# Performance work log

Measured on AMD Instinct MI355X. Metric: run time of the kernel, lower is better.

Reference implementation:

```python
import jax, jax.numpy as jnp
import numpy as np

B, T, J, E, H = 32, 120, 24, 128, 8
d = E // H           # attention_dim = 16
D = J * E            # input_dim = 3072
FF = 256
NEG = -1e9


def _bn(x, g, b):
    # BatchNorm1d over channels-last layout: normalize each of D channels over (batch, time)
    m = x.mean(axis=(0, 1))
    v = x.var(axis=(0, 1))
    return (x - m) * jax.lax.rsqrt(v + 1e-5) * g + b


def setup_inputs() -> dict:
    key = jax.random.key(0)
    ks = jax.random.split(key, 12)
    s = 0.05  # keep activations well-scaled
    return {
        "src_seqs": jax.random.normal(ks[0], (B, T, D), jnp.float32),
        "Wq_t": jax.random.normal(ks[1], (H, J, d, E), jnp.float32) * s,
        "Wk_t": jax.random.normal(ks[2], (H, J, d, E), jnp.float32) * s,
        "Wv_t": jax.random.normal(ks[3], (H, J, d, E), jnp.float32) * s,
        "Wp_t": jax.random.normal(ks[4], (D, D), jnp.float32) * s,
        "bp_t": jnp.zeros((D,), jnp.float32),
        "g_t": jnp.ones((D,), jnp.float32),
        "b_t": jnp.zeros((D,), jnp.float32),
        "Wq_s": jax.random.normal(ks[5], (H, J, d, E), jnp.float32) * s,
        "Wk_s": jax.random.normal(ks[6], (H, d, E), jnp.float32) * s,
        "Wv_s": jax.random.normal(ks[7], (H, d, E), jnp.float32) * s,
        "Wp_s": jax.random.normal(ks[8], (D, D), jnp.float32) * s,
        "bp_s": jnp.zeros((D,), jnp.float32),
        "g_s": jnp.ones((D,), jnp.float32),
        "b_s": jnp.zeros((D,), jnp.float32),
        "W1": jax.random.normal(ks[9], (FF, D), jnp.float32) * s,
        "b1": jnp.zeros((FF,), jnp.float32),
        "W2": jax.random.normal(ks[10], (D, FF), jnp.float32) * s,
        "b2": jnp.zeros((D,), jnp.float32),
        "g_f": jnp.ones((D,), jnp.float32),
        "b_f": jnp.zeros((D,), jnp.float32),
    }


def reference(src_seqs, Wq_t, Wk_t, Wv_t, Wp_t, bp_t, g_t, b_t,
              Wq_s, Wk_s, Wv_s, Wp_s, bp_s, g_s, b_s,
              W1, b1, W2, b2, g_f, b_f):
    Bz, Tz, Dz = src_seqs.shape
    x = src_seqs.reshape(Bz, Tz, J, E)  # per-joint embeddings
    sc = 1.0 / jnp.sqrt(jnp.float32(d))

    # ---- temporal attention (per head h, per joint j; causal over time) ----
    q = jnp.einsum('btje,hjde->bhjtd', x, Wq_t)
    k = jnp.einsum('btje,hjde->bhjtd', x, Wk_t)
    v = jnp.einsum('btje,hjde->bhjtd', x, Wv_t)
    causal = jnp.where(jnp.tril(jnp.ones((Tz, Tz), bool)), 0.0, NEG)
    a = jax.nn.softmax(jnp.einsum('bhjtd,bhjsd->bhjts', q, k) * sc + causal, axis=-1)
    ta = jnp.einsum('bhjts,bhjsd->bhjtd', a, v)
    # concat order: heads outer, joints inner -> (b,t,h,j,d)
    ta = ta.transpose(0, 3, 1, 2, 4).reshape(Bz, Tz, Dz)
    ta = ta @ Wp_t.T + bp_t
    ta = _bn(ta + src_seqs, g_t, b_t)  # dropout=identity (eval)

    # ---- spatial attention (per head h; attends over joints, shared K/V proj) ----
    qs = jnp.einsum('btje,hjde->bhtjd', x, Wq_s)
    ks = jnp.einsum('btje,hde->bhtjd', x, Wk_s)
    vs = jnp.einsum('btje,hde->bhtjd', x, Wv_s)
    asft = jax.nn.softmax(jnp.einsum('bhtjd,bhtkd->bhtjk', qs, ks) * sc, axis=-1)
    sa = jnp.einsum('bhtjk,bhtkd->bhtjd', asft, vs)
    sa = sa.transpose(0, 2, 1, 3, 4).reshape(Bz, Tz, Dz)  # (b,t,h,j,d)
    sa = sa @ Wp_s.T + bp_s
    sa = _bn(sa + src_seqs, g_s, b_s)

    # ---- feed-forward + residual + norm ----
    att = ta + sa
    h1 = jax.nn.relu(att @ W1.T + b1)
    out = _bn((h1 @ W2.T + b2) + att, g_f, b_f)
    return out
```

## Files before the change

kernel.cpp:

```cpp
#include <hip/hip_runtime.h>

typedef unsigned short u16;
typedef __bf16 bf16x8 __attribute__((ext_vector_type(8)));
typedef float f4 __attribute__((ext_vector_type(4)));
typedef float float4v __attribute__((ext_vector_type(4)));
typedef u16 u16x4 __attribute__((ext_vector_type(4)));

#define NX 11796480
#define LDP 136

__device__ __forceinline__ float bf2f(u16 u){ __bf16 h = __builtin_bit_cast(__bf16, u); return (float)h; }
__device__ __forceinline__ u16 f2bf(float f){ __bf16 h = (__bf16)f; return __builtin_bit_cast(u16, h); }

__device__ __forceinline__ void gload_lds16(const u16* g, u16* l){
  __builtin_amdgcn_global_load_lds((const __attribute__((address_space(1))) void*)g,
                                   (__attribute__((address_space(3))) void*)l, 16, 0, 0);
}

__device__ __forceinline__ void cvt4seg(const float* __restrict__ in, u16* __restrict__ out, int i){
  float4v v = *(const float4v*)&in[i*4];
  u16x4 o;
  o[0]=f2bf(v[0]); o[1]=f2bf(v[1]); o[2]=f2bf(v[2]); o[3]=f2bf(v[3]);
  *(u16x4*)&out[i*4] = o;
}

__global__ void k_prep(const float* __restrict__ src, u16* __restrict__ x_bf,
                       const float* __restrict__ wpt, u16* __restrict__ wptb,
                       const float* __restrict__ wps, u16* __restrict__ wpsb,
                       const float* __restrict__ w1,  u16* __restrict__ w1b,
                       const float* __restrict__ w2,  u16* __restrict__ w2b,
                       const float* __restrict__ wqt, const float* __restrict__ wkt,
                       const float* __restrict__ wvt, const float* __restrict__ wqs,
                       const float* __restrict__ wks, const float* __restrict__ wvs,
                       u16* __restrict__ wcat, float* __restrict__ accs){
  int i = blockIdx.x*256 + threadIdx.x;
  if (i < 18432){ accs[i] = 0.f; return; }
  i -= 18432;
  if (i < 2949120){ cvt4seg(src, x_bf, i); return; }
  i -= 2949120;
  if (i < 2359296){ cvt4seg(wpt, wptb, i); return; }
  i -= 2359296;
  if (i < 2359296){ cvt4seg(wps, wpsb, i); return; }
  i -= 2359296;
  if (i < 196608){ cvt4seg(w1, w1b, i); return; }
  i -= 196608;
  if (i < 196608){ cvt4seg(w2, w2b, i); return; }
  i -= 196608;
  int e = i & 127;
  int n = (i >> 7) % 768;
  int j = i / (768*128);
  float v;
  if (n < 512){
    int tn = n >> 7, hh = (n >> 4) & 7, dd = n & 15;
    const float* W = (tn==0)? wqt : (tn==1)? wkt : (tn==2)? wvt : wqs;
    v = W[(((hh*24 + j)*16 + dd) << 7) + e];
  } else {
    int m = n - 512;
    int tn = m >> 7, hh = (m >> 4) & 7, dd = m & 15;
    const float* W = (tn==0)? wks : wvs;
    v = W[((hh*16 + dd) << 7) + e];
  }
  wcat[i] = f2bf(v);
}

__device__ __forceinline__ void gemm_tile(const u16* __restrict__ Ab, int lda,
                                          const u16* __restrict__ Bb, int ldb,
                                          int K, f4 acc[4][4], u16* As, u16* Bs)
{
  const int tid  = threadIdx.x;
  const int lane = tid & 63;
  const int wid  = tid >> 6;
  const int waveM = (wid >> 1) * 64;
  const int waveN = (wid & 1) * 64;
  const int quad = lane >> 4;
  const int r16  = lane & 15;
  const int srow = tid >> 3;
  const int gcol = ((tid & 7) ^ (srow & 7)) * 8;

  #pragma unroll
  for (int mt=0; mt<4; mt++)
    #pragma unroll
    for (int nt=0; nt<4; nt++)
      #pragma unroll
      for (int q=0; q<4; q++) acc[mt][nt][q] = 0.f;

  for (int k0 = 0; k0 < K; k0 += 64){
    __syncthreads();
    #pragma unroll
    for (int i=0; i<4; i++){
      int row = srow + i*32;
      gload_lds16(&Ab[(size_t)row*lda + k0 + gcol], As + wid*512 + i*2048);
      gload_lds16(&Bb[(size_t)row*ldb + k0 + gcol], Bs + wid*512 + i*2048);
    }
    __builtin_amdgcn_s_waitcnt(0);
    __syncthreads();
    #pragma unroll
    for (int kk=0; kk<2; kk++){
      bf16x8 af[4], bfr[4];
      const int soff = ((kk*4 + quad) ^ (r16 & 7)) * 8;
      #pragma unroll
      for (int mt=0; mt<4; mt++)
        af[mt] = *(const bf16x8*)&As[(waveM + mt*16 + r16)*64 + soff];
      #pragma unroll
      for (int nt=0; nt<4; nt++)
        bfr[nt] = *(const bf16x8*)&Bs[(waveN + nt*16 + r16)*64 + soff];
      #pragma unroll
      for (int mt=0; mt<4; mt++)
        #pragma unroll
        for (int nt=0; nt<4; nt++)
          acc[mt][nt] = __builtin_amdgcn_mfma_f32_16x16x32_bf16(af[mt], bfr[nt], acc[mt][nt], 0, 0, 0);
    }
  }
  __syncthreads();
}

__global__ __launch_bounds__(256)
void gemm_qkv(const u16* __restrict__ x, const u16* __restrict__ wcat,
              u16* __restrict__ qt, u16* __restrict__ kt, u16* __restrict__ vt,
              u16* __restrict__ qs, u16* __restrict__ ks, u16* __restrict__ vs)
{
  __shared__ __align__(16) u16 As[128*128];
  __shared__ __align__(16) u16 Bs[128*128];
  int m0 = blockIdx.x*128, j = blockIdx.y;
  const u16* Ab = x + (size_t)m0*3072 + j*128;
  const u16* Bbase = wcat + (size_t)j*98304;
  int tid = threadIdx.x, lane = tid & 63, wid = tid >> 6;
  int quad = lane >> 4, r16 = lane & 15;
  int srow16 = tid >> 4;
  int cslot  = tid & 15;
  int gcol   = (cslot ^ srow16) * 8;

  #pragma unroll
  for (int it=0; it<8; it++){
    int row = srow16 + it*16;
    gload_lds16(&Ab[(size_t)row*3072 + gcol], As + tid*8 + it*2048);
  }

  int waveM = (wid>>1)*64, waveN = (wid&1)*64;

  for (int nc=0; nc<6; nc++){
    const u16* Bb = Bbase + (size_t)(nc*128)*128;
    #pragma unroll
    for (int it=0; it<8; it++){
      int row = srow16 + it*16;
      gload_lds16(&Bb[(size_t)row*128 + gcol], Bs + tid*8 + it*2048);
    }
    __builtin_amdgcn_s_waitcnt(0);
    __syncthreads();

    f4 acc[4][4];
    #pragma unroll
    for (int mt=0; mt<4; mt++)
      #pragma unroll
      for (int nt=0; nt<4; nt++)
        #pragma unroll
        for (int q=0; q<4; q++) acc[mt][nt][q] = 0.f;

    #pragma unroll
    for (int kk=0; kk<4; kk++){
      bf16x8 af[4], bfr[4];
      const int soff = ((kk*4 + quad) ^ r16) * 8;
      #pragma unroll
      for (int mt=0; mt<4; mt++)
        af[mt] = *(const bf16x8*)&As[(waveM + mt*16 + r16)*128 + soff];
      #pragma unroll
      for (int nt=0; nt<4; nt++)
        bfr[nt] = *(const bf16x8*)&Bs[(waveN + nt*16 + r16)*128 + soff];
      #pragma unroll
      for (int mt=0; mt<4; mt++)
        #pragma unroll
        for (int nt=0; nt<4; nt++)
          acc[mt][nt] = __builtin_amdgcn_mfma_f32_16x16x32_bf16(af[mt], bfr[nt], acc[mt][nt], 0, 0, 0);
    }

    #pragma unroll
    for (int mt=0; mt<4; mt++){
      #pragma unroll
      for (int reg=0; reg<4; reg++){
        int row = m0 + waveM + mt*16 + quad*4 + reg;
        int b = row / 120, t = row % 120;
        #pragma unroll
        for (int nt=0; nt<4; nt++){
          int n = nc*128 + waveN + nt*16 + r16;
          u16 uv = f2bf(acc[mt][nt][reg]);
          if (n < 384){
            int tn = n >> 7, hh = (n >> 4) & 7, dd = n & 15;
            u16* base = (tn==0)? qt : (tn==1)? kt : vt;
            base[((((size_t)(b*8+hh)*24 + j)*120 + t) << 4) + dd] = uv;
          } else {
            int m2 = n - 384;
            int tn = m2 >> 7, hh = (m2 >> 4) & 7, dd = m2 & 15;
            u16* base = (tn==0)? qs : (tn==1)? ks : vs;
            base[((((size_t)row*8 + hh)*24 + j) << 4) + dd] = uv;
          }
        }
      }
    }
    __syncthreads();
  }
}


__device__ __forceinline__ void stageA384(const u16* __restrict__ g, int kcol,
                                          u16* __restrict__ slotA, int lane, int wid){
  #pragma unroll
  for (int i=0;i<2;i++){
    int row = wid*32 + i*16 + (lane>>2);
    int sw  = (((lane & 3) ^ ((lane>>3) & 3)) << 3);
    gload_lds16(&g[(size_t)row*3072 + kcol + sw], slotA + (wid*2+i)*512);
  }
}
__device__ __forceinline__ void stageB384(const u16* __restrict__ g, int kcol,
                                          u16* __restrict__ slotB, int lane, int wid){
  #pragma unroll
  for (int i=0;i<3;i++){
    int row = wid*48 + i*16 + (lane>>2);
    int sw  = (((lane & 3) ^ ((lane>>3) & 3)) << 3);
    gload_lds16(&g[(size_t)row*3072 + kcol + sw], slotB + (wid*3+i)*512);
  }
}

__global__ __launch_bounds__(512, 2)
void gemm_proj384(const u16* __restrict__ A0, const u16* __restrict__ B0, const float* __restrict__ b0,
                  const u16* __restrict__ A1, const u16* __restrict__ B1, const float* __restrict__ b1v,
                  const u16* __restrict__ resb, u16* __restrict__ O0, u16* __restrict__ O1,
                  float* __restrict__ st0, float* __restrict__ st1)
{
  __shared__ __align__(16) u16 smem[61440];
  const int tid = threadIdx.x, lane = tid & 63, wid = tid >> 6;
  const int quad = lane >> 4, r16 = lane & 15;
  const int wm = wid >> 2, wn = wid & 3;

  int lin = blockIdx.x + 15*blockIdx.y + 120*blockIdx.z;
  int nidx = (lin & 7)*30 + (lin >> 3);
  int zz = nidx / 120; int rem = nidx - zz*120;
  int by = rem / 15, bx = rem - by*15;

  const int m0 = bx*256, n0 = by*384;
  const u16* Ag = (zz ? A1 : A0) + (size_t)m0*3072;
  const u16* Bg = (zz ? B1 : B0) + (size_t)n0*3072;
  const float* bias = zz ? b1v : b0;
  u16* out = zz ? O1 : O0;
  float* stp = zz ? st1 : st0;

  const int soff = ((quad ^ ((r16>>1)&3)) << 3);
  const int arow = wm*128 + r16;
  const int brow = wn*96 + r16;

  f4 acc[8][6];
  #pragma unroll
  for (int i=0;i<8;i++)
    #pragma unroll
    for (int n=0;n<6;n++)
      #pragma unroll
      for (int q=0;q<4;q++) acc[i][n][q] = 0.f;

  u16* Sa = smem;
  u16* Sb = smem + 20480;
  u16* Sc = smem + 40960;

  stageA384(Ag, 0,  Sa,        lane, wid);
  stageB384(Bg, 0,  Sa + 8192, lane, wid);
  stageA384(Ag, 32, Sb,        lane, wid);
  stageB384(Bg, 32, Sb + 8192, lane, wid);
  asm volatile("s_waitcnt vmcnt(5)" ::: "memory");
  __builtin_amdgcn_s_barrier();

  const int NT = 96;
  bf16x8 af[4], bf[6];

  for (int t=0; t<NT; ++t){
    const int kc2 = ((t+2 < NT) ? (t+2) : 0) * 32;

    #pragma unroll
    for (int i=0;i<4;i++) af[i] = *(const bf16x8*)&Sa[(arow + i*16)*32 + soff];
    #pragma unroll
    for (int n=0;n<6;n++) bf[n] = *(const bf16x8*)&Sa[8192 + (brow + n*16)*32 + soff];
    stageA384(Ag, kc2, Sc, lane, wid);
    __builtin_amdgcn_s_setprio(1);
    #pragma unroll
    for (int i=0;i<4;i++)
      #pragma unroll
      for (int n=0;n<6;n++)
        acc[i][n] = __builtin_amdgcn_mfma_f32_16x16x32_bf16(af[i], bf[n], acc[i][n], 0,0,0);
    __builtin_amdgcn_s_setprio(0);

    #pragma unroll
    for (int i=0;i<4;i++) af[i] = *(const bf16x8*)&Sa[(arow + 64 + i*16)*32 + soff];
    stageB384(Bg, kc2, Sc + 8192, lane, wid);
    __builtin_amdgcn_s_setprio(1);
    #pragma unroll
    for (int i=0;i<4;i++)
      #pragma unroll
      for (int n=0;n<6;n++)
        acc[4+i][n] = __builtin_amdgcn_mfma_f32_16x16x32_bf16(af[i], bf[n], acc[4+i][n], 0,0,0);
    __builtin_amdgcn_s_setprio(0);

    asm volatile("s_waitcnt vmcnt(5)" ::: "memory");
    __builtin_amdgcn_s_barrier();
    u16* tp = Sa; Sa = Sb; Sb = Sc; Sc = tp;
  }
  asm volatile("s_waitcnt vmcnt(0)" ::: "memory");

  float bv[6];
  #pragma unroll
  for (int n=0;n<6;n++) bv[n] = bias[n0 + wn*96 + n*16 + r16];
  float s[6] = {0,0,0,0,0,0}, s2[6] = {0,0,0,0,0,0};
  #pragma unroll
  for (int mf=0; mf<8; mf++){
    #pragma unroll
    for (int reg=0; reg<4; reg++){
      int grow = m0 + wm*128 + mf*16 + quad*4 + reg;
      #pragma unroll
      for (int n=0;n<6;n++){
        int gcol = n0 + wn*96 + n*16 + r16;
        size_t idx = (size_t)grow*3072 + gcol;
        float v = acc[mf][n][reg] + bv[n] + bf2f(resb[idx]);
        out[idx] = f2bf(v);
        s[n] += v; s2[n] += v*v;
      }
    }
  }
  #pragma unroll
  for (int n=0;n<6;n++){
    float a = s[n], b = s2[n];
    a += __shfl_xor(a, 16); a += __shfl_xor(a, 32);
    b += __shfl_xor(b, 16); b += __shfl_xor(b, 32);
    if (quad == 0){
      int col = n0 + wn*96 + n*16 + r16;
      atomicAdd(&stp[col], a);
      atomicAdd(&stp[3072 + col], b);
    }
  }
}

__global__ __launch_bounds__(256)
void gemm_ff2(const u16* __restrict__ A, const u16* __restrict__ B, const float* __restrict__ bias,
              const u16* __restrict__ resb, u16* __restrict__ out, float* __restrict__ stp)
{
  __shared__ __align__(16) u16 As[128*64];
  __shared__ __align__(16) u16 Bs[128*64];
  int m0 = blockIdx.x*128, n0 = blockIdx.y*128;
  f4 acc[4][4];
  gemm_tile(A + (size_t)m0*256, 256, B + (size_t)n0*256, 256, 256, acc, As, Bs);
  int lane = threadIdx.x & 63, wid = threadIdx.x >> 6;
  int waveM = (wid>>1)*64, waveN = (wid&1)*64;
  int quad = lane>>4, r16 = lane&15;
  float s[4] = {0,0,0,0}, s2[4] = {0,0,0,0};
  #pragma unroll
  for (int mt=0; mt<4; mt++){
    #pragma unroll
    for (int reg=0; reg<4; reg++){
      int grow = m0 + waveM + mt*16 + quad*4 + reg;
      #pragma unroll
      for (int nt=0; nt<4; nt++){
        int gcol = n0 + waveN + nt*16 + r16;
        size_t idx = (size_t)grow*3072 + gcol;
        float v = acc[mt][nt][reg] + bias[gcol] + bf2f(resb[idx]);
        out[idx] = f2bf(v);
        s[nt] += v; s2[nt] += v*v;
      }
    }
  }
  #pragma unroll
  for (int nt=0; nt<4; nt++){
    float a = s[nt], b = s2[nt];
    a += __shfl_xor(a, 16); a += __shfl_xor(a, 32);
    b += __shfl_xor(b, 16); b += __shfl_xor(b, 32);
    if (quad == 0){
      int col = n0 + waveN + nt*16 + r16;
      atomicAdd(&stp[col], a);
      atomicAdd(&stp[3072 + col], b);
    }
  }
}

__global__ __launch_bounds__(256)
void gemm_relu(const u16* __restrict__ A, const u16* __restrict__ B, int K, int N,
               const float* __restrict__ bias, u16* __restrict__ out)
{
  __shared__ __align__(16) u16 As[128*64];
  __shared__ __align__(16) u16 Bs[128*64];
  int m0 = blockIdx.x*128, n0 = blockIdx.y*128;
  f4 acc[4][4];
  gemm_tile(A + (size_t)m0*K, K, B + (size_t)n0*K, K, K, acc, As, Bs);
  int lane = threadIdx.x & 63, wid = threadIdx.x >> 6;
  int waveM = (wid>>1)*64, waveN = (wid&1)*64;
  int quad = lane>>4, r16 = lane&15;
  #pragma unroll
  for (int mt=0; mt<4; mt++){
    #pragma unroll
    for (int reg=0; reg<4; reg++){
      int grow = m0 + waveM + mt*16 + quad*4 + reg;
      #pragma unroll
      for (int nt=0; nt<4; nt++){
        int gcol = n0 + waveN + nt*16 + r16;
        float v = acc[mt][nt][reg] + bias[gcol];
        out[(size_t)grow*N + gcol] = f2bf(v > 0.f ? v : 0.f);
      }
    }
  }
}

__global__ __launch_bounds__(256)
void attn_both(const u16* __restrict__ qt, const u16* __restrict__ kt,
               const u16* __restrict__ vt, u16* __restrict__ ta,
               const u16* __restrict__ qsp, const u16* __restrict__ ksp,
               const u16* __restrict__ vsp, u16* __restrict__ sa)
{
  __shared__ __align__(16) char smem[39168];
  int tid = threadIdx.x, lane = tid & 63, wid = tid >> 6;
  int quad = lane >> 4, r16 = lane & 15;

  if (blockIdx.x < 6144){
    u16* P  = (u16*)smem;
    u16* Vt = (u16*)(smem + 34816);
    int blk = blockIdx.x;
    int b = blk / 192;
    int rem = blk % 192;
    int h = rem / 24, j = rem % 24;
    const u16* qb = qt + (size_t)blk*1920;
    const u16* kb = kt + (size_t)blk*1920;
    const u16* vb = vt + (size_t)blk*1920;

    for (int e = tid; e < 1920; e += 256){
      int s = e >> 4, dd = e & 15;
      Vt[dd*LDP + s] = vb[e];
    }
    if (tid < 128){ int dd = tid >> 3, s = 120 + (tid & 7); Vt[dd*LDP + s] = 0; }
    __syncthreads();

    bf16x8 zv;
    #pragma unroll
    for (int i=0;i<8;i++) zv[i] = (__bf16)0.f;

    const int m0 = wid * 32;
    bf16x8 qf[2];
    #pragma unroll
    for (int mt=0; mt<2; mt++){
      int row = m0 + mt*16 + r16; if (row > 119) row = 119;
      qf[mt] = (quad < 2) ? *(const bf16x8*)&qb[row*16 + (quad&1)*8] : zv;
    }

    f4 S[2][8];
    #pragma unroll
    for (int nt=0; nt<8; nt++){
      int col = nt*16 + r16; int colc = col > 119 ? 119 : col;
      bf16x8 kf = (quad < 2) ? *(const bf16x8*)&kb[colc*16 + (quad&1)*8] : zv;
      #pragma unroll
      for (int mt=0; mt<2; mt++){
        f4 zz = {0.f, 0.f, 0.f, 0.f};
        S[mt][nt] = __builtin_amdgcn_mfma_f32_16x16x32_bf16(qf[mt], kf, zz, 0, 0, 0);
      }
    }

    #pragma unroll
    for (int mt=0; mt<2; mt++)
      #pragma unroll
      for (int nt=0; nt<8; nt++)
        #pragma unroll
        for (int reg=0; reg<4; reg++){
          int c = nt*16 + r16;
          int r = m0 + mt*16 + quad*4 + reg;
          float v = S[mt][nt][reg] * 0.25f;
          S[mt][nt][reg] = (c > r || c >= 120) ? -1e30f : v;
        }

    float Zr[2][4];
    #pragma unroll
    for (int mt=0; mt<2; mt++)
      #pragma unroll
      for (int reg=0; reg<4; reg++){
        float m = -1e30f;
        #pragma unroll
        for (int nt=0; nt<8; nt++) m = fmaxf(m, S[mt][nt][reg]);
        #pragma unroll
        for (int off=1; off<16; off<<=1) m = fmaxf(m, __shfl_xor(m, off, 16));
        float z = 0.f;
        #pragma unroll
        for (int nt=0; nt<8; nt++){
          float e = __expf(S[mt][nt][reg] - m);
          S[mt][nt][reg] = e;
          z += e;
        }
        #pragma unroll
        for (int off=1; off<16; off<<=1) z += __shfl_xor(z, off, 16);
        Zr[mt][reg] = z;
      }

    #pragma unroll
    for (int mt=0; mt<2; mt++)
      #pragma unroll
      for (int nt=0; nt<8; nt++)
        #pragma unroll
        for (int reg=0; reg<4; reg++)
          P[(m0 + mt*16 + quad*4 + reg)*LDP + nt*16 + r16] = f2bf(S[mt][nt][reg]);
    __syncthreads();

    f4 O[2];
    #pragma unroll
    for (int mt=0; mt<2; mt++){ O[mt][0]=0.f; O[mt][1]=0.f; O[mt][2]=0.f; O[mt][3]=0.f; }
    #pragma unroll
    for (int kt8=0; kt8<4; kt8++){
      bf16x8 vf = *(const bf16x8*)&Vt[r16*LDP + kt8*32 + quad*8];
      #pragma unroll
      for (int mt=0; mt<2; mt++){
        bf16x8 pf = *(const bf16x8*)&P[(m0 + mt*16 + r16)*LDP + kt8*32 + quad*8];
        O[mt] = __builtin_amdgcn_mfma_f32_16x16x32_bf16(pf, vf, O[mt], 0, 0, 0);
      }
    }

    #pragma unroll
    for (int mt=0; mt<2; mt++)
      #pragma unroll
      for (int reg=0; reg<4; reg++){
        int r = m0 + mt*16 + quad*4 + reg;
        if (r < 120){
          size_t idx = (size_t)(b*120 + r)*3072 + h*384 + j*16 + r16;
          ta[idx] = f2bf(O[mt][reg] / Zr[mt][reg]);
        }
      }
  } else {
    float* Ks = (float*)smem;
    float* Vs = (float*)(smem + 12288);
    int bt = blockIdx.x - 6144;
    size_t base = (size_t)bt * 3072;
    for (int c = tid; c < 384; c += 256){
      bf16x8 kv = *(const bf16x8*)&ksp[base + c*8];
      bf16x8 vv = *(const bf16x8*)&vsp[base + c*8];
      #pragma unroll
      for (int i=0;i<8;i++){ Ks[c*8+i] = (float)kv[i]; Vs[c*8+i] = (float)vv[i]; }
    }
    __syncthreads();
    if (tid < 192){
      int h = tid / 24, j = tid % 24;
      float q[16];
      #pragma unroll
      for (int d2=0; d2<16; d2++) q[d2] = bf2f(qsp[base + h*384 + j*16 + d2]);
      float sc[24], mx = -1e30f;
      #pragma unroll
      for (int kk=0; kk<24; kk++){
        float dot = 0.f;
        #pragma unroll
        for (int d2=0; d2<16; d2++) dot += q[d2]*Ks[h*384 + kk*16 + d2];
        sc[kk] = dot * 0.25f;
        mx = fmaxf(mx, sc[kk]);
      }
      float Z = 0.f, acc[16];
      #pragma unroll
      for (int d2=0; d2<16; d2++) acc[d2] = 0.f;
      #pragma unroll
      for (int kk=0; kk<24; kk++){
        float w = __expf(sc[kk] - mx);
        Z += w;
        #pragma unroll
        for (int d2=0; d2<16; d2++) acc[d2] += w*Vs[h*384 + kk*16 + d2];
      }
      float inv = 1.f / Z;
      #pragma unroll
      for (int d2=0; d2<16; d2++) sa[base + h*384 + j*16 + d2] = f2bf(acc[d2]*inv);
    }
  }
}

__global__ void bn_coef2(const float* __restrict__ accT, const float* __restrict__ gT,
                         const float* __restrict__ bT, float* __restrict__ cT,
                         const float* __restrict__ accS, const float* __restrict__ gS,
                         const float* __restrict__ bS, float* __restrict__ cS){
  int isS = blockIdx.x >= 12;
  const float* acc = isS ? accS : accT;
  const float* g   = isS ? gS : gT;
  const float* b   = isS ? bS : bT;
  float* coef      = isS ? cS : cT;
  int c = (blockIdx.x % 12)*256 + threadIdx.x;
  float mean = acc[c] * (1.f/3840.f);
  float var  = acc[3072+c] * (1.f/3840.f) - mean*mean;
  float sc = g[c] * rsqrtf(var + 1e-5f);
  coef[c] = sc;
  coef[3072+c] = b[c] - mean*sc;
}

__global__ void bn_coef(const float* __restrict__ acc, const float* __restrict__ g,
                        const float* __restrict__ b, float* __restrict__ coef){
  int c = blockIdx.x*256 + threadIdx.x;
  float mean = acc[c] * (1.f/3840.f);
  float var  = acc[3072+c] * (1.f/3840.f) - mean*mean;
  float sc = g[c] * rsqrtf(var + 1e-5f);
  coef[c] = sc;
  coef[3072+c] = b[c] - mean*sc;
}

__global__ void bn_apply2(const u16* __restrict__ Ytb, const u16* __restrict__ Ysb,
                          const float* __restrict__ ct, const float* __restrict__ cs,
                          u16* __restrict__ attB){
  int i = blockIdx.x*256 + threadIdx.x;
  int c = (i*4) % 3072;
  u16x4 yt = *(const u16x4*)&Ytb[i*4];
  u16x4 ys = *(const u16x4*)&Ysb[i*4];
  u16x4 o;
  #pragma unroll
  for (int k=0;k<4;k++){
    float a = bf2f(yt[k])*ct[c+k] + ct[3072+c+k] + bf2f(ys[k])*cs[c+k] + cs[3072+c+k];
    o[k] = f2bf(a);
  }
  *(u16x4*)&attB[i*4] = o;
}

__global__ void bn_out(const u16* __restrict__ Yfb, const float* __restrict__ cf,
                       float* __restrict__ out){
  int i = blockIdx.x*256 + threadIdx.x;
  int c = (i*4) % 3072;
  u16x4 yf = *(const u16x4*)&Yfb[i*4];
  float4v o;
  #pragma unroll
  for (int k=0;k<4;k++) o[k] = bf2f(yf[k])*cf[c+k] + cf[3072+c+k];
  *(float4v*)&out[i*4] = o;
}

extern "C" void kernel_launch(void* const* d_in, const int* in_sizes, int n_in,
                              void* d_out, int out_size, void* d_ws, size_t ws_size,
                              hipStream_t stream)
{
  const float* src  = (const float*)d_in[0];
  const float* Wq_t = (const float*)d_in[1];
  const float* Wk_t = (const float*)d_in[2];
  const float* Wv_t = (const float*)d_in[3];
  const float* Wp_t = (const float*)d_in[4];
  const float* bp_t = (const float*)d_in[5];
  const float* g_t  = (const float*)d_in[6];
  const float* b_t  = (const float*)d_in[7];
  const float* Wq_s = (const float*)d_in[8];
  const float* Wk_s = (const float*)d_in[9];
  const float* Wv_s = (const float*)d_in[10];
  const float* Wp_s = (const float*)d_in[11];
  const float* bp_s = (const float*)d_in[12];
  const float* g_s  = (const float*)d_in[13];
  const float* b_s  = (const float*)d_in[14];
  const float* W1   = (const float*)d_in[15];
  const float* b1   = (const float*)d_in[16];
  const float* W2   = (const float*)d_in[17];
  const float* b2   = (const float*)d_in[18];
  const float* g_f  = (const float*)d_in[19];
  const float* b_f  = (const float*)d_in[20];

  char* ws = (char*)d_ws;
  u16* x_bf  = (u16*)(ws + 0ull);
  u16* wptb  = (u16*)(ws + 23592960ull);
  u16* wpsb  = (u16*)(ws + 42467328ull);
  u16* w1b   = (u16*)(ws + 61341696ull);
  u16* w2b   = (u16*)(ws + 62914560ull);
  u16* wcat  = (u16*)(ws + 64487424ull);
  u16* qt    = (u16*)(ws + 69206016ull);
  u16* kt    = qt + NX;
  u16* vt    = kt + NX;
  u16* qs    = vt + NX;
  u16* ks    = qs + NX;
  u16* vs    = ks + NX;
  u16* tab   = (u16*)(ws + 210763776ull);
  u16* sab   = (u16*)(ws + 234356736ull);
  float* accT = (float*)(ws + 257949696ull);
  float* accS = accT + 6144;
  float* accF = accS + 6144;
  float* cT   = accF + 6144;
  float* cS   = cT + 6144;
  float* cF   = cS + 6144;
  u16* Ytb  = qt;
  u16* Ysb  = kt;
  u16* attB = vt;
  u16* Yfb  = qs;
  u16* h1   = wcat;
  float* out = (float*)d_out;

  k_prep<<<40776, 256, 0, stream>>>(src, x_bf, Wp_t, wptb, Wp_s, wpsb, W1, w1b, W2, w2b,
                                    Wq_t, Wk_t, Wv_t, Wq_s, Wk_s, Wv_s, wcat, accT);
  gemm_qkv<<<dim3(30,24), 256, 0, stream>>>(x_bf, wcat, qt, kt, vt, qs, ks, vs);
  attn_both<<<9984, 256, 0, stream>>>(qt, kt, vt, tab, qs, ks, vs, sab);
  gemm_proj384<<<dim3(15,8,2), 512, 0, stream>>>(tab, wptb, bp_t, sab, wpsb, bp_s,
                                                 x_bf, Ytb, Ysb, accT, accS);
  bn_coef2<<<24, 256, 0, stream>>>(accT, g_t, b_t, cT, accS, g_s, b_s, cS);
  bn_apply2<<<11520, 256, 0, stream>>>(Ytb, Ysb, cT, cS, attB);
  gemm_relu<<<dim3(30,2), 256, 0, stream>>>(attB, w1b, 3072, 256, b1, h1);
  gemm_ff2<<<dim3(30,24), 256, 0, stream>>>(h1, w2b, b2, attB, Yfb, accF);
  bn_coef<<<12, 256, 0, stream>>>(accF, g_f, b_f, cF);
  bn_out<<<11520, 256, 0, stream>>>(Yfb, cF, out);
}
```

Before: 604.0 us.

## Retile FF1 GEMM to 32-row tiles with triple-buffered async LDS staging

The first feed-forward GEMM (M=3840, N=256, K=3072) ran on only 60 blocks. It now uses 32x128 tiles across 240 blocks, with a three-slot LDS ring fed by direct global-to-LDS loads, XOR-swizzled columns and a prefetch distance of two. The attention kernel's V transpose also now loads 8 bf16 values per thread with a vector load instead of scalar loads. The cost is less data reuse per block and a fixed K of 3072 hardcoded into the kernel.

```diff
diff --git a/kernel.cpp b/kernel.cpp
--- a/kernel.cpp
+++ b/kernel.cpp
@@ -375,29 +375,93 @@
   }
 }
 
+__device__ __forceinline__ void stageR_A(const u16* __restrict__ g, int kc, u16* __restrict__ slot,
+                                         int tid, int srow, int gcol){
+  gload_lds16(&g[(size_t)srow*3072 + kc + gcol], slot + tid*8);
+}
+__device__ __forceinline__ void stageR_B(const u16* __restrict__ g, int kc, u16* __restrict__ slot,
+                                         int tid, int srow, int gcol){
+  #pragma unroll
+  for (int i=0;i<4;i++)
+    gload_lds16(&g[(size_t)(srow + i*32)*3072 + kc + gcol], slot + 2048 + i*2048 + tid*8);
+}
+
 __global__ __launch_bounds__(256)
-void gemm_relu(const u16* __restrict__ A, const u16* __restrict__ B, int K, int N,
+void gemm_relu(const u16* __restrict__ A, const u16* __restrict__ B,
                const float* __restrict__ bias, u16* __restrict__ out)
 {
-  __shared__ __align__(16) u16 As[128*64];
-  __shared__ __align__(16) u16 Bs[128*64];
-  int m0 = blockIdx.x*128, n0 = blockIdx.y*128;
-  f4 acc[4][4];
-  gemm_tile(A + (size_t)m0*K, K, B + (size_t)n0*K, K, K, acc, As, Bs);
-  int lane = threadIdx.x & 63, wid = threadIdx.x >> 6;
-  int waveM = (wid>>1)*64, waveN = (wid&1)*64;
-  int quad = lane>>4, r16 = lane&15;
-  #pragma unroll
-  for (int mt=0; mt<4; mt++){
+  __shared__ __align__(16) u16 smem[30720];
+  const int tid = threadIdx.x, lane = tid & 63, wid = tid >> 6;
+  const int quad = lane >> 4, r16 = lane & 15;
+  const int waveM = (wid >> 1) * 16, waveN = (wid & 1) * 64;
+  const int m0 = blockIdx.x * 32, n0 = blockIdx.y * 128;
+  const u16* Ag = A + (size_t)m0 * 3072;
+  const u16* Bg = B + (size_t)n0 * 3072;
+
+  const int srow = tid >> 3;
+  const int gcol = ((tid & 7) ^ (srow & 7)) * 8;
+
+  f4 acc[4];
+  #pragma unroll
+  for (int n=0;n<4;n++)
+    #pragma unroll
+    for (int q=0;q<4;q++) acc[n][q] = 0.f;
+
+  u16* Sa = smem;
+  u16* Sb = smem + 10240;
+  u16* Sc = smem + 20480;
+
+  stageR_A(Ag, 0,  Sa, tid, srow, gcol);
+  stageR_B(Bg, 0,  Sa, tid, srow, gcol);
+  stageR_A(Ag, 64, Sb, tid, srow, gcol);
+  stageR_B(Bg, 64, Sb, tid, srow, gcol);
+  asm volatile("s_waitcnt vmcnt(5)" ::: "memory");
+  __builtin_amdgcn_s_barrier();
+
+  const int NT = 48;
+  const int s0 = (quad ^ (r16 & 7)) * 8;
+  const int s1 = ((4 + quad) ^ (r16 & 7)) * 8;
+
+  for (int t=0; t<NT; ++t){
+    const int kc2 = ((t+2 < NT) ? (t+2) : 0) * 64;
+
+    bf16x8 a0 = *(const bf16x8*)&Sa[(waveM + r16)*64 + s0];
+    bf16x8 b0[4];
+    #pragma unroll
+    for (int n=0;n<4;n++) b0[n] = *(const bf16x8*)&Sa[2048 + (waveN + n*16 + r16)*64 + s0];
+    stageR_A(Ag, kc2, Sc, tid, srow, gcol);
+    __builtin_amdgcn_s_setprio(1);
+    #pragma unroll
+    for (int n=0;n<4;n++)
+      acc[n] = __builtin_amdgcn_mfma_f32_16x16x32_bf16(a0, b0[n], acc[n], 0,0,0);
+    __builtin_amdgcn_s_setprio(0);
+
+    bf16x8 a1 = *(const bf16x8*)&Sa[(waveM + r16)*64 + s1];
+    bf16x8 b1[4];
+    #pragma unroll
+    for (int n=0;n<4;n++) b1[n] = *(const bf16x8*)&Sa[2048 + (waveN + n*16 + r16)*64 + s1];
+    stageR_B(Bg, kc2, Sc, tid, srow, gcol);
+    __builtin_amdgcn_s_setprio(1);
+    #pragma unroll
+    for (int n=0;n<4;n++)
+      acc[n] = __builtin_amdgcn_mfma_f32_16x16x32_bf16(a1, b1[n], acc[n], 0,0,0);
+    __builtin_amdgcn_s_setprio(0);
+
+    asm volatile("s_waitcnt vmcnt(5)" ::: "memory");
+    __builtin_amdgcn_s_barrier();
+    u16* tp = Sa; Sa = Sb; Sb = Sc; Sc = tp;
+  }
+  asm volatile("s_waitcnt vmcnt(0)" ::: "memory");
+
+  #pragma unroll
+  for (int n=0;n<4;n++){
+    int gcolo = n0 + waveN + n*16 + r16;
+    float bv = bias[gcolo];
     #pragma unroll
     for (int reg=0; reg<4; reg++){
-      int grow = m0 + waveM + mt*16 + quad*4 + reg;
-      #pragma unroll
-      for (int nt=0; nt<4; nt++){
-        int gcol = n0 + waveN + nt*16 + r16;
-        float v = acc[mt][nt][reg] + bias[gcol];
-        out[(size_t)grow*N + gcol] = f2bf(v > 0.f ? v : 0.f);
-      }
+      int grow = m0 + waveM + quad*4 + reg;
+      float v = acc[n][reg] + bv;
+      out[(size_t)grow*256 + gcolo] = f2bf(v > 0.f ? v : 0.f);
     }
   }
 }
@@ -423,9 +487,11 @@
     const u16* kb = kt + (size_t)blk*1920;
     const u16* vb = vt + (size_t)blk*1920;
 
-    for (int e = tid; e < 1920; e += 256){
-      int s = e >> 4, dd = e & 15;
-      Vt[dd*LDP + s] = vb[e];
+    if (tid < 240){
+      int s = tid >> 1, hf = (tid & 1) * 8;
+      bf16x8 vv = *(const bf16x8*)&vb[s*16 + hf];
+      #pragma unroll
+      for (int q=0;q<8;q++) Vt[(hf + q)*LDP + s] = __builtin_bit_cast(u16, (__bf16)vv[q]);
     }
     if (tid < 128){ int dd = tid >> 3, s = 120 + (tid & 7); Vt[dd*LDP + s] = 0; }
     __syncthreads();
@@ -679,7 +745,7 @@
                                                  x_bf, Ytb, Ysb, accT, accS);
   bn_coef2<<<24, 256, 0, stream>>>(accT, g_t, b_t, cT, accS, g_s, b_s, cS);
   bn_apply2<<<11520, 256, 0, stream>>>(Ytb, Ysb, cT, cS, attB);
-  gemm_relu<<<dim3(30,2), 256, 0, stream>>>(attB, w1b, 3072, 256, b1, h1);
+  gemm_relu<<<dim3(120,2), 256, 0, stream>>>(attB, w1b, b1, h1);
   gemm_ff2<<<dim3(30,24), 256, 0, stream>>>(h1, w2b, b2, attB, Yfb, accF);
   bn_coef<<<12, 256, 0, stream>>>(accF, g_f, b_f, cF);
   bn_out<<<11520, 256, 0, stream>>>(Yfb, cF, out);
```

Measured after the change: 558.7 us. 1.08x faster.
